# Optimization experiments

Measured on AMD Instinct MI355X. Metric: run time of the kernel, lower is better.

The kernel has to match this reference:

```python
import jax, jax.numpy as jnp
import numpy as np

N = 100000   # nodes
E = 1600000  # edges (before self-loops)
D = 128      # input_dim
H = 128      # hidden_dim


def setup_inputs() -> dict:
    key = jax.random.key(0)
    ks = jax.random.split(key, 10)
    def lin_w(k, fan_in, fan_out):
        return jax.random.normal(k, (fan_in, fan_out), jnp.float32) / np.float32(np.sqrt(fan_in))
    x = jax.random.normal(ks[0], (N, D), jnp.float32)
    edge_index = jax.random.randint(ks[1], (2, E), 0, N)
    return {
        "x": x,
        "edge_index": edge_index,
        "W0": lin_w(ks[2], D, H), "b0": jnp.zeros((H,), jnp.float32),
        "W1": lin_w(ks[3], H, H), "b1": jnp.zeros((H,), jnp.float32),
        "W2": lin_w(ks[4], H, H), "b2": jnp.zeros((H,), jnp.float32),
        "Wr": lin_w(ks[5], D, H), "br": jnp.zeros((H,), jnp.float32),
    }


def _gcn_norm(edge_index, n):
    # add self-loops, then symmetric normalization D^{-1/2} (A+I) D^{-1/2}
    loop = jnp.arange(n, dtype=edge_index.dtype)
    src = jnp.concatenate([edge_index[0], loop])
    dst = jnp.concatenate([edge_index[1], loop])
    deg = jax.ops.segment_sum(jnp.ones_like(src, dtype=jnp.float32), dst, num_segments=n)
    dinv = jnp.where(deg > 0, jax.lax.rsqrt(deg), 0.0)
    norm = dinv[src] * dinv[dst]  # [E+N]
    return src, dst, norm


def _gcn_layer(x, W, b, src, dst, norm, n):
    h = x @ W                      # [n, H] dense GEMM
    msg = h[src] * norm[:, None]   # gather + scale  [E+N, H]
    out = jax.ops.segment_sum(msg, dst, num_segments=n)  # scatter-add
    return out + b


def reference(x, edge_index, W0, b0, W1, b1, W2, b2, Wr, br):
    n = x.shape[0]
    src, dst, norm = _gcn_norm(edge_index, n)
    residual = x @ Wr + br
    # layer 0: GCN -> relu -> (dropout=identity, eval) -> +residual
    h = jax.nn.relu(_gcn_layer(x, W0, b0, src, dst, norm, n)) + residual
    # layer 1
    h = jax.nn.relu(_gcn_layer(h, W1, b1, src, dst, norm, n))
    # layer 2
    h = jax.nn.relu(_gcn_layer(h, W2, b2, src, dst, norm, n))
    return h
```

## Files before the change

kernel.cpp:

```cpp
#include <hip/hip_runtime.h>
#include <hip/hip_bf16.h>
#include <cstdint>


#define WS_ALIGN(x) (((x) + 255) & ~(size_t)255)

typedef __bf16 bf16x8 __attribute__((ext_vector_type(8)));
typedef float  floatx4 __attribute__((ext_vector_type(4)));

static __device__ __forceinline__ float bf_lo(unsigned u) {
  return __builtin_bit_cast(float, u << 16);
}
static __device__ __forceinline__ float bf_hi(unsigned u) {
  return __builtin_bit_cast(float, u & 0xffff0000u);
}
static __device__ __forceinline__ unsigned short f2bs(float f) {
  unsigned u = __builtin_bit_cast(unsigned, f);
  return (unsigned short)((u + 0x7fffu + ((u >> 16) & 1u)) >> 16);
}
static __device__ __forceinline__ unsigned pack2(float a, float b) {
  return (unsigned)f2bs(a) | ((unsigned)f2bs(b) << 16);
}

__global__ void k_prep(const float* __restrict__ x, unsigned* __restrict__ xb, int n4,
                       int* __restrict__ cnt, int n,
                       const float* __restrict__ W0, const float* __restrict__ W1,
                       const float* __restrict__ W2, const float* __restrict__ Wr,
                       unsigned short* __restrict__ Wt, int zb, int xbn) {
  int b = blockIdx.x;
  if (b < zb) {
    int i = b * 256 + threadIdx.x;
    if (i < n) cnt[i] = 0;
  } else if (b < zb + xbn) {
    int i = (b - zb) * 256 + threadIdx.x;
    if (i < n4) {
      float4 v = ((const float4*)x)[i];
      uint2 o;
      o.x = pack2(v.x, v.y);
      o.y = pack2(v.z, v.w);
      ((uint2*)xb)[i] = o;
    }
  } else {
    int wb = b - zb - xbn;
    int mat = wb >> 6, blk = wb & 63;
    const float* W = mat == 0 ? W0 : mat == 1 ? W1 : mat == 2 ? W2 : Wr;
    unsigned short* T = Wt + (size_t)mat * 16384;
    int i = blk * 256 + threadIdx.x;
    int k = i >> 7, nn = i & 127;
    T[nn * 128 + k] = f2bs(W[i]);
  }
}

__global__ void k_count(const int* __restrict__ dst, int E,
                        int* __restrict__ cnt, int* __restrict__ pos) {
  int e = blockIdx.x * blockDim.x + threadIdx.x;
  if (e < E) pos[e] = atomicAdd(&cnt[dst[e]], 1);
}

__global__ __launch_bounds__(1024) void k_scan1(const int* __restrict__ cnt, int n,
                                                int* __restrict__ rs, int* __restrict__ bsum,
                                                float* __restrict__ dinv) {
  __shared__ int tmp[1024];
  int tid = threadIdx.x;
  int i = blockIdx.x * 1024 + tid;
  int v = (i < n) ? cnt[i] : 0;
  if (i < n) dinv[i] = rsqrtf((float)(v + 1));
  int vp = (v + 7) & ~7;
  tmp[tid] = vp;
  __syncthreads();
  for (int off = 1; off < 1024; off <<= 1) {
    int t = (tid >= off) ? tmp[tid - off] : 0;
    __syncthreads();
    tmp[tid] += t;
    __syncthreads();
  }
  if (i < n) rs[i] = tmp[tid] - vp;
  if (tid == 1023) bsum[blockIdx.x] = tmp[1023];
}

__global__ __launch_bounds__(128) void k_scan2(int* bsum, int nb) {
  __shared__ int tmp[128];
  int tid = threadIdx.x;
  int v = (tid < nb) ? bsum[tid] : 0;
  tmp[tid] = v;
  __syncthreads();
  for (int off = 1; off < 128; off <<= 1) {
    int t = (tid >= off) ? tmp[tid - off] : 0;
    __syncthreads();
    tmp[tid] += t;
    __syncthreads();
  }
  if (tid < nb) bsum[tid] = tmp[tid] - v;
}

__global__ void k_fill(const int* __restrict__ src, const int* __restrict__ dst, int E,
                       const int* __restrict__ rs, const int* __restrict__ bsum,
                       const int* __restrict__ pos, const int* __restrict__ cnt,
                       const float* __restrict__ dinv,
                       int2* __restrict__ epk, int n) {
  int e = blockIdx.x * blockDim.x + threadIdx.x;
  if (e < E) {
    int s = src[e], d = dst[e];
    int idx = rs[d] + bsum[d >> 10] + pos[e];
    int2 v;
    v.x = s;
    v.y = __float_as_int(dinv[s] * dinv[d]);
    epk[idx] = v;
  } else if (e - E < n) {
    int node = e - E;
    int c = cnt[node];
    int cp = (c + 7) & ~7;
    int base = rs[node] + bsum[node >> 10];
    int2 z; z.x = 0; z.y = 0;
    for (int k = base + c; k < base + cp; k++) epk[k] = z;
  }
}

__global__ __launch_bounds__(256, 2) void k_gemm_mfma(
    const unsigned short* __restrict__ Xb,
    const unsigned short* __restrict__ Wt,
    const float* __restrict__ bias,
    unsigned short* __restrict__ Y,
    int n) {
  __shared__ unsigned short sWt[128 * 128];
  {
    const uint4* s4 = (const uint4*)Wt;
    uint4* d4 = (uint4*)sWt;
    for (int i = threadIdx.x; i < 2048; i += 256) d4[i] = s4[i];
  }
  __syncthreads();

  const int lane = threadIdx.x & 63;
  const int wave = threadIdx.x >> 6;
  const int l15 = lane & 15;
  const int quad = lane >> 4;
  const int rbase = blockIdx.x * 64 + wave * 16;

  const bf16x8* sW8 = (const bf16x8*)sWt;
  bf16x8 b[8][4];
#pragma unroll
  for (int ct = 0; ct < 8; ct++)
#pragma unroll
    for (int kc = 0; kc < 4; kc++)
      b[ct][kc] = sW8[(ct * 16 + l15) * 16 + kc * 4 + quad];

  int row = rbase + l15;
  row = row < n ? row : n - 1;
  const bf16x8* X8 = (const bf16x8*)Xb;
  bf16x8 a[4];
#pragma unroll
  for (int kc = 0; kc < 4; kc++)
    a[kc] = X8[(size_t)row * 16 + kc * 4 + quad];

  floatx4 acc[8];
#pragma unroll
  for (int ct = 0; ct < 8; ct++) acc[ct] = (floatx4){0.f, 0.f, 0.f, 0.f};

#pragma unroll
  for (int kc = 0; kc < 4; kc++)
#pragma unroll
    for (int ct = 0; ct < 8; ct++)
      acc[ct] = __builtin_amdgcn_mfma_f32_16x16x32_bf16(a[kc], b[ct][kc], acc[ct], 0, 0, 0);

  const int orow = rbase + quad * 4;
#pragma unroll
  for (int ct = 0; ct < 8; ct++) {
    const int c = ct * 16 + l15;
    const float bv = bias ? bias[c] : 0.f;
#pragma unroll
    for (int r4 = 0; r4 < 4; r4++) {
      int r = orow + r4;
      if (r < n) Y[(size_t)r * 128 + c] = f2bs(acc[ct][r4] + bv);
    }
  }
}

static __device__ __forceinline__ void fma8(float wgt, uint4 h, float* a) {
  a[0] = fmaf(wgt, bf_lo(h.x), a[0]);
  a[1] = fmaf(wgt, bf_hi(h.x), a[1]);
  a[2] = fmaf(wgt, bf_lo(h.y), a[2]);
  a[3] = fmaf(wgt, bf_hi(h.y), a[3]);
  a[4] = fmaf(wgt, bf_lo(h.z), a[4]);
  a[5] = fmaf(wgt, bf_hi(h.z), a[5]);
  a[6] = fmaf(wgt, bf_lo(h.w), a[6]);
  a[7] = fmaf(wgt, bf_hi(h.w), a[7]);
}

__global__ __launch_bounds__(256, 4) void k_agg(
    const uint4* __restrict__ H,
    const int* __restrict__ rs,
    const int* __restrict__ bsum,
    const int* __restrict__ cnt,
    const int2* __restrict__ epk,
    const float* __restrict__ dinv,
    const float* __restrict__ bias,
    const uint4* __restrict__ resid,
    uint4* __restrict__ outb,
    float4* __restrict__ outf,
    int n) {
  int node = blockIdx.x * 16 + (threadIdx.x >> 4);
  int l = threadIdx.x & 15;
  if (node >= n) return;

  float di = dinv[node];
  float ws = di * di;
  uint4 hv = H[(size_t)node * 16 + l];
  float a[8];
  a[0] = bf_lo(hv.x) * ws; a[1] = bf_hi(hv.x) * ws;
  a[2] = bf_lo(hv.y) * ws; a[3] = bf_hi(hv.y) * ws;
  a[4] = bf_lo(hv.z) * ws; a[5] = bf_hi(hv.z) * ws;
  a[6] = bf_lo(hv.w) * ws; a[7] = bf_hi(hv.w) * ws;

  int beg = rs[node] + bsum[node >> 10];
  int pdeg = (cnt[node] + 7) & ~7;
  const int4* epk4 = (const int4*)epk;

  for (int j = 0; j < pdeg; j += 8) {
    int b2 = (beg + j) >> 1;
    int4 e0 = epk4[b2 + 0];
    int4 e1 = epk4[b2 + 1];
    int4 e2 = epk4[b2 + 2];
    int4 e3 = epk4[b2 + 3];
    uint4 h0 = H[(size_t)(unsigned)e0.x * 16 + l];
    uint4 h1 = H[(size_t)(unsigned)e0.z * 16 + l];
    uint4 h2 = H[(size_t)(unsigned)e1.x * 16 + l];
    uint4 h3 = H[(size_t)(unsigned)e1.z * 16 + l];
    uint4 h4 = H[(size_t)(unsigned)e2.x * 16 + l];
    uint4 h5 = H[(size_t)(unsigned)e2.z * 16 + l];
    uint4 h6 = H[(size_t)(unsigned)e3.x * 16 + l];
    uint4 h7 = H[(size_t)(unsigned)e3.z * 16 + l];
    fma8(__int_as_float(e0.y), h0, a);
    fma8(__int_as_float(e0.w), h1, a);
    fma8(__int_as_float(e1.y), h2, a);
    fma8(__int_as_float(e1.w), h3, a);
    fma8(__int_as_float(e2.y), h4, a);
    fma8(__int_as_float(e2.w), h5, a);
    fma8(__int_as_float(e3.y), h6, a);
    fma8(__int_as_float(e3.w), h7, a);
  }

  float4 bl = ((const float4*)bias)[l * 2];
  float4 bh = ((const float4*)bias)[l * 2 + 1];
  a[0] = fmaxf(a[0] + bl.x, 0.f); a[1] = fmaxf(a[1] + bl.y, 0.f);
  a[2] = fmaxf(a[2] + bl.z, 0.f); a[3] = fmaxf(a[3] + bl.w, 0.f);
  a[4] = fmaxf(a[4] + bh.x, 0.f); a[5] = fmaxf(a[5] + bh.y, 0.f);
  a[6] = fmaxf(a[6] + bh.z, 0.f); a[7] = fmaxf(a[7] + bh.w, 0.f);
  if (resid) {
    uint4 r = resid[(size_t)node * 16 + l];
    a[0] += bf_lo(r.x); a[1] += bf_hi(r.x);
    a[2] += bf_lo(r.y); a[3] += bf_hi(r.y);
    a[4] += bf_lo(r.z); a[5] += bf_hi(r.z);
    a[6] += bf_lo(r.w); a[7] += bf_hi(r.w);
  }
  if (outb) {
    uint4 o;
    o.x = pack2(a[0], a[1]); o.y = pack2(a[2], a[3]);
    o.z = pack2(a[4], a[5]); o.w = pack2(a[6], a[7]);
    outb[(size_t)node * 16 + l] = o;
  } else {
    float4 o0; o0.x = a[0]; o0.y = a[1]; o0.z = a[2]; o0.w = a[3];
    float4 o1; o1.x = a[4]; o1.y = a[5]; o1.z = a[6]; o1.w = a[7];
    outf[(size_t)node * 32 + l * 2] = o0;
    outf[(size_t)node * 32 + l * 2 + 1] = o1;
  }
}

extern "C" void kernel_launch(void* const* d_in, const int* in_sizes, int n_in,
                              void* d_out, int out_size, void* d_ws, size_t ws_size,
                              hipStream_t stream) {
  const float* x  = (const float*)d_in[0];
  const int* edges = (const int*)d_in[1];
  const float* W0 = (const float*)d_in[2];
  const float* b0 = (const float*)d_in[3];
  const float* W1 = (const float*)d_in[4];
  const float* b1 = (const float*)d_in[5];
  const float* W2 = (const float*)d_in[6];
  const float* b2 = (const float*)d_in[7];
  const float* Wr = (const float*)d_in[8];
  const float* br = (const float*)d_in[9];

  int N = in_sizes[0] / 128;
  int E = in_sizes[1] / 2;
  const int* src = edges;
  const int* dst = edges + E;

  char* ws = (char*)d_ws;
  size_t off = 0;
  auto alloc = [&](size_t bytes) -> void* {
    void* p = ws + off; off = WS_ALIGN(off + bytes); return p;
  };
  int*   cnt    = (int*)  alloc((size_t)N * 4);
  float* dinv   = (float*)alloc((size_t)N * 4);
  int*   rs     = (int*)  alloc((size_t)(N + 1) * 4);
  int*   bsum   = (int*)  alloc(1024);
  int2*  epk    = (int2*) alloc(((size_t)E + 8 * (size_t)N) * 8);
  unsigned short* xb = (unsigned short*)alloc((size_t)N * 128 * 2);
  unsigned short* Wt = (unsigned short*)alloc((size_t)4 * 16384 * 2);
  unsigned short* A  = (unsigned short*)alloc((size_t)N * 128 * 2);
  unsigned short* Hb = (unsigned short*)alloc((size_t)N * 128 * 2);
  unsigned short* R  = (unsigned short*)alloc((size_t)N * 128 * 2);
  int* pos = (int*)A;
  (void)ws_size; (void)n_in; (void)out_size;

  int nb1 = (N + 1023) / 1024;

  int n4 = N * 128 / 4;
  int zb = (N + 255) / 256;
  int xbn = (n4 + 255) / 256;
  k_prep <<<zb + xbn + 256, 256, 0, stream>>>(x, (unsigned*)xb, n4, cnt, N,
                                              W0, W1, W2, Wr, Wt, zb, xbn);
  k_count<<<(E + 255) / 256, 256, 0, stream>>>(dst, E, cnt, pos);
  k_scan1<<<nb1, 1024, 0, stream>>>(cnt, N, rs, bsum, dinv);
  k_scan2<<<1, 128, 0, stream>>>(bsum, nb1);
  k_fill <<<(E + N + 255) / 256, 256, 0, stream>>>(src, dst, E, rs, bsum, pos,
                                                   cnt, dinv, epk, N);

  int gb = (N + 63) / 64;
  int ab = (N + 15) / 16;

  unsigned short* Wt0 = Wt;
  unsigned short* Wt1 = Wt + 16384;
  unsigned short* Wt2 = Wt + 2 * 16384;
  unsigned short* Wtr = Wt + 3 * 16384;

  k_gemm_mfma<<<gb, 256, 0, stream>>>(xb, Wtr, br, R, N);
  k_gemm_mfma<<<gb, 256, 0, stream>>>(xb, Wt0, nullptr, A, N);
  k_agg<<<ab, 256, 0, stream>>>((const uint4*)A, rs, bsum, cnt, epk, dinv, b0,
                                (const uint4*)R, (uint4*)Hb, nullptr, N);
  k_gemm_mfma<<<gb, 256, 0, stream>>>(Hb, Wt1, nullptr, A, N);
  k_agg<<<ab, 256, 0, stream>>>((const uint4*)A, rs, bsum, cnt, epk, dinv, b1,
                                nullptr, (uint4*)R, nullptr, N);
  k_gemm_mfma<<<gb, 256, 0, stream>>>(R, Wt2, nullptr, A, N);
  k_agg<<<ab, 256, 0, stream>>>((const uint4*)A, rs, bsum, cnt, epk, dinv, b2,
                                nullptr, nullptr, (float4*)d_out, N);
}
```

Baseline: 526.4 us.

## Privatize per-XCC degree counters to avoid cross-die atomic contention in CSR build

The edge-count kernel now reads the hardware XCC id and increments one of eight per-XCC copies of the destination counters with workgroup-scope relaxed atomics. It stores the rank together with the XCC id in pos. The scan kernel folds the eight copies into per-XCC offsets and a total degree. The fill kernel combines these to place each edge. The intent is to keep counting atomics inside each XCC's L2 and avoid device-coherent traffic, at the cost of eight times the counter memory (aliased onto the Hb buffer) plus the extra scan and fill reads; the workgroup-scope atomic is only correct if L2 coherence within an XCC holds across workgroups.

```diff
diff --git a/kernel.cpp b/kernel.cpp
--- a/kernel.cpp
+++ b/kernel.cpp
@@ -23,14 +23,14 @@
 }
 
 __global__ void k_prep(const float* __restrict__ x, unsigned* __restrict__ xb, int n4,
-                       int* __restrict__ cnt, int n,
+                       int* __restrict__ cnt8, int nz,
                        const float* __restrict__ W0, const float* __restrict__ W1,
                        const float* __restrict__ W2, const float* __restrict__ Wr,
                        unsigned short* __restrict__ Wt, int zb, int xbn) {
   int b = blockIdx.x;
   if (b < zb) {
     int i = b * 256 + threadIdx.x;
-    if (i < n) cnt[i] = 0;
+    if (i < nz) cnt8[i] = 0;
   } else if (b < zb + xbn) {
     int i = (b - zb) * 256 + threadIdx.x;
     if (i < n4) {
@@ -52,26 +52,46 @@
 }
 
 __global__ void k_count(const int* __restrict__ dst, int E,
-                        int* __restrict__ cnt, int* __restrict__ pos) {
+                        int* __restrict__ cnt8, int* __restrict__ pos, int NP) {
+  unsigned xcc = __builtin_amdgcn_s_getreg(6164);
+  int r = xcc & 7;
   int e = blockIdx.x * blockDim.x + threadIdx.x;
-  if (e < E) pos[e] = atomicAdd(&cnt[dst[e]], 1);
-}
-
-__global__ __launch_bounds__(1024) void k_scan1(const int* __restrict__ cnt, int n,
+  if (e < E) {
+    int d = dst[e];
+    int rank = __hip_atomic_fetch_add(&cnt8[(size_t)r * NP + d], 1,
+                                      __ATOMIC_RELAXED, __HIP_MEMORY_SCOPE_WORKGROUP);
+    pos[e] = (rank << 3) | r;
+  }
+}
+
+__global__ __launch_bounds__(1024) void k_scan1(int* __restrict__ cnt8, int n, int NP,
                                                 int* __restrict__ rs, int* __restrict__ bsum,
-                                                float* __restrict__ dinv) {
+                                                float* __restrict__ dinv,
+                                                int* __restrict__ tot) {
   __shared__ int tmp[1024];
   int tid = threadIdx.x;
   int i = blockIdx.x * 1024 + tid;
-  int v = (i < n) ? cnt[i] : 0;
-  if (i < n) dinv[i] = rsqrtf((float)(v + 1));
-  int vp = (v + 7) & ~7;
+  int t = 0;
+  if (i < n) {
+    int run = 0;
+#pragma unroll
+    for (int r = 0; r < 8; r++) {
+      size_t idx = (size_t)r * NP + i;
+      int c = cnt8[idx];
+      cnt8[idx] = run;
+      run += c;
+    }
+    t = run;
+    tot[i] = t;
+    dinv[i] = rsqrtf((float)(t + 1));
+  }
+  int vp = (t + 7) & ~7;
   tmp[tid] = vp;
   __syncthreads();
   for (int off = 1; off < 1024; off <<= 1) {
-    int t = (tid >= off) ? tmp[tid - off] : 0;
+    int tv = (tid >= off) ? tmp[tid - off] : 0;
     __syncthreads();
-    tmp[tid] += t;
+    tmp[tid] += tv;
     __syncthreads();
   }
   if (i < n) rs[i] = tmp[tid] - vp;
@@ -95,20 +115,22 @@
 
 __global__ void k_fill(const int* __restrict__ src, const int* __restrict__ dst, int E,
                        const int* __restrict__ rs, const int* __restrict__ bsum,
-                       const int* __restrict__ pos, const int* __restrict__ cnt,
+                       const int* __restrict__ pos, const int* __restrict__ cnt8,
+                       const int* __restrict__ tot, int NP,
                        const float* __restrict__ dinv,
                        int2* __restrict__ epk, int n) {
   int e = blockIdx.x * blockDim.x + threadIdx.x;
   if (e < E) {
     int s = src[e], d = dst[e];
-    int idx = rs[d] + bsum[d >> 10] + pos[e];
+    int pr = pos[e];
+    int idx = rs[d] + bsum[d >> 10] + cnt8[(size_t)(pr & 7) * NP + d] + (pr >> 3);
     int2 v;
     v.x = s;
     v.y = __float_as_int(dinv[s] * dinv[d]);
     epk[idx] = v;
   } else if (e - E < n) {
     int node = e - E;
-    int c = cnt[node];
+    int c = tot[node];
     int cp = (c + 7) & ~7;
     int base = rs[node] + bsum[node >> 10];
     int2 z; z.x = 0; z.y = 0;
@@ -190,7 +212,7 @@
     const uint4* __restrict__ H,
     const int* __restrict__ rs,
     const int* __restrict__ bsum,
-    const int* __restrict__ cnt,
+    const int* __restrict__ tot,
     const int2* __restrict__ epk,
     const float* __restrict__ dinv,
     const float* __restrict__ bias,
@@ -212,7 +234,7 @@
   a[6] = bf_lo(hv.w) * ws; a[7] = bf_hi(hv.w) * ws;
 
   int beg = rs[node] + bsum[node >> 10];
-  int pdeg = (cnt[node] + 7) & ~7;
+  int pdeg = (tot[node] + 7) & ~7;
   const int4* epk4 = (const int4*)epk;
 
   for (int j = 0; j < pdeg; j += 8) {
@@ -289,7 +311,7 @@
   auto alloc = [&](size_t bytes) -> void* {
     void* p = ws + off; off = WS_ALIGN(off + bytes); return p;
   };
-  int*   cnt    = (int*)  alloc((size_t)N * 4);
+  int*   tot    = (int*)  alloc((size_t)N * 4);
   float* dinv   = (float*)alloc((size_t)N * 4);
   int*   rs     = (int*)  alloc((size_t)(N + 1) * 4);
   int*   bsum   = (int*)  alloc(1024);
@@ -300,20 +322,23 @@
   unsigned short* Hb = (unsigned short*)alloc((size_t)N * 128 * 2);
   unsigned short* R  = (unsigned short*)alloc((size_t)N * 128 * 2);
   int* pos = (int*)A;
+  int NP = (N + 15) & ~15;
+  int* cnt8 = (int*)Hb;
+  int nz = 8 * NP;
   (void)ws_size; (void)n_in; (void)out_size;
 
   int nb1 = (N + 1023) / 1024;
 
   int n4 = N * 128 / 4;
-  int zb = (N + 255) / 256;
+  int zb = (nz + 255) / 256;
   int xbn = (n4 + 255) / 256;
-  k_prep <<<zb + xbn + 256, 256, 0, stream>>>(x, (unsigned*)xb, n4, cnt, N,
+  k_prep <<<zb + xbn + 256, 256, 0, stream>>>(x, (unsigned*)xb, n4, cnt8, nz,
                                               W0, W1, W2, Wr, Wt, zb, xbn);
-  k_count<<<(E + 255) / 256, 256, 0, stream>>>(dst, E, cnt, pos);
-  k_scan1<<<nb1, 1024, 0, stream>>>(cnt, N, rs, bsum, dinv);
+  k_count<<<(E + 255) / 256, 256, 0, stream>>>(dst, E, cnt8, pos, NP);
+  k_scan1<<<nb1, 1024, 0, stream>>>(cnt8, N, NP, rs, bsum, dinv, tot);
   k_scan2<<<1, 128, 0, stream>>>(bsum, nb1);
   k_fill <<<(E + N + 255) / 256, 256, 0, stream>>>(src, dst, E, rs, bsum, pos,
-                                                   cnt, dinv, epk, N);
+                                                   cnt8, tot, NP, dinv, epk, N);
 
   int gb = (N + 63) / 64;
   int ab = (N + 15) / 16;
@@ -325,12 +350,12 @@
 
   k_gemm_mfma<<<gb, 256, 0, stream>>>(xb, Wtr, br, R, N);
   k_gemm_mfma<<<gb, 256, 0, stream>>>(xb, Wt0, nullptr, A, N);
-  k_agg<<<ab, 256, 0, stream>>>((const uint4*)A, rs, bsum, cnt, epk, dinv, b0,
+  k_agg<<<ab, 256, 0, stream>>>((const uint4*)A, rs, bsum, tot, epk, dinv, b0,
                                 (const uint4*)R, (uint4*)Hb, nullptr, N);
   k_gemm_mfma<<<gb, 256, 0, stream>>>(Hb, Wt1, nullptr, A, N);
-  k_agg<<<ab, 256, 0, stream>>>((const uint4*)A, rs, bsum, cnt, epk, dinv, b1,
+  k_agg<<<ab, 256, 0, stream>>>((const uint4*)A, rs, bsum, tot, epk, dinv, b1,
                                 nullptr, (uint4*)R, nullptr, N);
   k_gemm_mfma<<<gb, 256, 0, stream>>>(R, Wt2, nullptr, A, N);
-  k_agg<<<ab, 256, 0, stream>>>((const uint4*)A, rs, bsum, cnt, epk, dinv, b2,
+  k_agg<<<ab, 256, 0, stream>>>((const uint4*)A, rs, bsum, tot, epk, dinv, b2,
                                 nullptr, nullptr, (float4*)d_out, N);
 }
```

Result: no change. 527.3 us (+0.2%).

## Replace CSR build with fixed-slot adjacency plus overflow list and prescaled features

Applied to the files above, without the earlier changes.

Replaces the count/scan/fill CSR construction with a single atomic pass that writes each edge's source into a 32-slot per-node array, spilling extra edges to a global overflow list. The symmetric normalization is factored: the GEMM epilogue scales each row by dinv[src] and the aggregation applies dinv[dst] at the end, so edges store only indices and the inner loop becomes plain adds. Padding slots point at a zeroed dummy row N. This removes three launches and the 8-byte edge records, but high-degree nodes linearly scan the whole overflow list, and neighbor order now depends on atomic ordering.

```diff
diff --git a/kernel.cpp b/kernel.cpp
--- a/kernel.cpp
+++ b/kernel.cpp
@@ -26,7 +26,9 @@
                        int* __restrict__ cnt, int n,
                        const float* __restrict__ W0, const float* __restrict__ W1,
                        const float* __restrict__ W2, const float* __restrict__ Wr,
-                       unsigned short* __restrict__ Wt, int zb, int xbn) {
+                       unsigned short* __restrict__ Wt,
+                       unsigned short* __restrict__ A, int* __restrict__ ovfn,
+                       int zb, int xbn) {
   int b = blockIdx.x;
   if (b < zb) {
     int i = b * 256 + threadIdx.x;
@@ -42,77 +44,20 @@
     }
   } else {
     int wb = b - zb - xbn;
-    int mat = wb >> 6, blk = wb & 63;
-    const float* W = mat == 0 ? W0 : mat == 1 ? W1 : mat == 2 ? W2 : Wr;
-    unsigned short* T = Wt + (size_t)mat * 16384;
-    int i = blk * 256 + threadIdx.x;
-    int k = i >> 7, nn = i & 127;
-    T[nn * 128 + k] = f2bs(W[i]);
-  }
-}
-
-__global__ void k_count(const int* __restrict__ dst, int E,
-                        int* __restrict__ cnt, int* __restrict__ pos) {
-  int e = blockIdx.x * blockDim.x + threadIdx.x;
-  if (e < E) pos[e] = atomicAdd(&cnt[dst[e]], 1);
-}
-
-__global__ __launch_bounds__(1024) void k_scan1(const int* __restrict__ cnt, int n,
-                                                int* __restrict__ rs, int* __restrict__ bsum,
-                                                float* __restrict__ dinv) {
-  __shared__ int tmp[1024];
-  int tid = threadIdx.x;
-  int i = blockIdx.x * 1024 + tid;
-  int v = (i < n) ? cnt[i] : 0;
-  if (i < n) dinv[i] = rsqrtf((float)(v + 1));
-  int vp = (v + 7) & ~7;
-  tmp[tid] = vp;
-  __syncthreads();
-  for (int off = 1; off < 1024; off <<= 1) {
-    int t = (tid >= off) ? tmp[tid - off] : 0;
-    __syncthreads();
-    tmp[tid] += t;
-    __syncthreads();
-  }
-  if (i < n) rs[i] = tmp[tid] - vp;
-  if (tid == 1023) bsum[blockIdx.x] = tmp[1023];
-}
-
-__global__ __launch_bounds__(128) void k_scan2(int* bsum, int nb) {
-  __shared__ int tmp[128];
-  int tid = threadIdx.x;
-  int v = (tid < nb) ? bsum[tid] : 0;
-  tmp[tid] = v;
-  __syncthreads();
-  for (int off = 1; off < 128; off <<= 1) {
-    int t = (tid >= off) ? tmp[tid - off] : 0;
-    __syncthreads();
-    tmp[tid] += t;
-    __syncthreads();
-  }
-  if (tid < nb) bsum[tid] = tmp[tid] - v;
-}
-
-__global__ void k_fill(const int* __restrict__ src, const int* __restrict__ dst, int E,
-                       const int* __restrict__ rs, const int* __restrict__ bsum,
-                       const int* __restrict__ pos, const int* __restrict__ cnt,
-                       const float* __restrict__ dinv,
-                       int2* __restrict__ epk, int n) {
-  int e = blockIdx.x * blockDim.x + threadIdx.x;
-  if (e < E) {
-    int s = src[e], d = dst[e];
-    int idx = rs[d] + bsum[d >> 10] + pos[e];
-    int2 v;
-    v.x = s;
-    v.y = __float_as_int(dinv[s] * dinv[d]);
-    epk[idx] = v;
-  } else if (e - E < n) {
-    int node = e - E;
-    int c = cnt[node];
-    int cp = (c + 7) & ~7;
-    int base = rs[node] + bsum[node >> 10];
-    int2 z; z.x = 0; z.y = 0;
-    for (int k = base + c; k < base + cp; k++) epk[k] = z;
+    if (wb < 256) {
+      int mat = wb >> 6, blk = wb & 63;
+      const float* W = mat == 0 ? W0 : mat == 1 ? W1 : mat == 2 ? W2 : Wr;
+      unsigned short* T = Wt + (size_t)mat * 16384;
+      int i = blk * 256 + threadIdx.x;
+      int k = i >> 7, nn = i & 127;
+      T[nn * 128 + k] = f2bs(W[i]);
+    } else {
+      if (threadIdx.x < 16) {
+        uint4 z; z.x = 0; z.y = 0; z.z = 0; z.w = 0;
+        ((uint4*)(A + (size_t)n * 128))[threadIdx.x] = z;
+      }
+      if (threadIdx.x == 16) *ovfn = 0;
+    }
   }
 }
 
@@ -120,6 +65,7 @@
     const unsigned short* __restrict__ Xb,
     const unsigned short* __restrict__ Wt,
     const float* __restrict__ bias,
+    const float* __restrict__ dv,
     unsigned short* __restrict__ Y,
     int n) {
   __shared__ unsigned short sWt[128 * 128];
@@ -163,6 +109,12 @@
       acc[ct] = __builtin_amdgcn_mfma_f32_16x16x32_bf16(a[kc], b[ct][kc], acc[ct], 0, 0, 0);
 
   const int orow = rbase + quad * 4;
+  float4 dvv;
+  dvv.x = 1.f; dvv.y = 1.f; dvv.z = 1.f; dvv.w = 1.f;
+  if (dv) {
+    int od = orow < n ? orow : 0;
+    dvv = *(const float4*)(dv + od);
+  }
 #pragma unroll
   for (int ct = 0; ct < 8; ct++) {
     const int c = ct * 16 + l15;
@@ -170,81 +122,107 @@
 #pragma unroll
     for (int r4 = 0; r4 < 4; r4++) {
       int r = orow + r4;
-      if (r < n) Y[(size_t)r * 128 + c] = f2bs(acc[ct][r4] + bv);
-    }
-  }
-}
-
-static __device__ __forceinline__ void fma8(float wgt, uint4 h, float* a) {
-  a[0] = fmaf(wgt, bf_lo(h.x), a[0]);
-  a[1] = fmaf(wgt, bf_hi(h.x), a[1]);
-  a[2] = fmaf(wgt, bf_lo(h.y), a[2]);
-  a[3] = fmaf(wgt, bf_hi(h.y), a[3]);
-  a[4] = fmaf(wgt, bf_lo(h.z), a[4]);
-  a[5] = fmaf(wgt, bf_hi(h.z), a[5]);
-  a[6] = fmaf(wgt, bf_lo(h.w), a[6]);
-  a[7] = fmaf(wgt, bf_hi(h.w), a[7]);
+      float dm = r4 == 0 ? dvv.x : r4 == 1 ? dvv.y : r4 == 2 ? dvv.z : dvv.w;
+      if (r < n) Y[(size_t)r * 128 + c] = f2bs(acc[ct][r4] * dm + bv);
+    }
+  }
+}
+
+__global__ void k_fill1p(const int* __restrict__ srcv, const int* __restrict__ dstv,
+                         int E, int* __restrict__ cnt, int* __restrict__ epk,
+                         int2* __restrict__ ovf, int* __restrict__ ovfn) {
+  int e = blockIdx.x * blockDim.x + threadIdx.x;
+  if (e < E) {
+    int s = srcv[e], d = dstv[e];
+    int rank = atomicAdd(&cnt[d], 1);
+    if (rank < 32) {
+      epk[(size_t)d * 32 + rank] = s;
+    } else {
+      int o = atomicAdd(ovfn, 1);
+      if (o < E) {
+        int2 t; t.x = s; t.y = d;
+        ovf[o] = t;
+      }
+    }
+  }
+}
+
+__global__ void k_aux(const int* __restrict__ cnt, float* __restrict__ dinv,
+                      int* __restrict__ epk, int n) {
+  int i = blockIdx.x * 256 + threadIdx.x;
+  if (i < n) {
+    int c = cnt[i];
+    dinv[i] = rsqrtf((float)(c + 1));
+    int cm = c < 32 ? c : 32;
+    int cp = (cm + 7) & ~7;
+    for (int k = cm; k < cp; k++) epk[(size_t)i * 32 + k] = n;
+  }
+}
+
+static __device__ __forceinline__ void add8(uint4 h, float* a) {
+  a[0] += bf_lo(h.x); a[1] += bf_hi(h.x);
+  a[2] += bf_lo(h.y); a[3] += bf_hi(h.y);
+  a[4] += bf_lo(h.z); a[5] += bf_hi(h.z);
+  a[6] += bf_lo(h.w); a[7] += bf_hi(h.w);
 }
 
 __global__ __launch_bounds__(256, 4) void k_agg(
     const uint4* __restrict__ H,
-    const int* __restrict__ rs,
-    const int* __restrict__ bsum,
     const int* __restrict__ cnt,
-    const int2* __restrict__ epk,
+    const int* __restrict__ epk,
     const float* __restrict__ dinv,
     const float* __restrict__ bias,
     const uint4* __restrict__ resid,
     uint4* __restrict__ outb,
     float4* __restrict__ outf,
-    int n) {
+    const int2* __restrict__ ovf, const int* __restrict__ ovfn,
+    int n, int Ecap) {
   int node = blockIdx.x * 16 + (threadIdx.x >> 4);
   int l = threadIdx.x & 15;
   if (node >= n) return;
 
-  float di = dinv[node];
-  float ws = di * di;
+  int tot = cnt[node];
+  int cm = tot < 32 ? tot : 32;
+  int pdeg = (cm + 7) & ~7;
+
   uint4 hv = H[(size_t)node * 16 + l];
   float a[8];
-  a[0] = bf_lo(hv.x) * ws; a[1] = bf_hi(hv.x) * ws;
-  a[2] = bf_lo(hv.y) * ws; a[3] = bf_hi(hv.y) * ws;
-  a[4] = bf_lo(hv.z) * ws; a[5] = bf_hi(hv.z) * ws;
-  a[6] = bf_lo(hv.w) * ws; a[7] = bf_hi(hv.w) * ws;
-
-  int beg = rs[node] + bsum[node >> 10];
-  int pdeg = (cnt[node] + 7) & ~7;
-  const int4* epk4 = (const int4*)epk;
-
+  a[0] = bf_lo(hv.x); a[1] = bf_hi(hv.x);
+  a[2] = bf_lo(hv.y); a[3] = bf_hi(hv.y);
+  a[4] = bf_lo(hv.z); a[5] = bf_hi(hv.z);
+  a[6] = bf_lo(hv.w); a[7] = bf_hi(hv.w);
+
+  const int4* epk4 = (const int4*)(epk + (size_t)node * 32);
   for (int j = 0; j < pdeg; j += 8) {
-    int b2 = (beg + j) >> 1;
-    int4 e0 = epk4[b2 + 0];
-    int4 e1 = epk4[b2 + 1];
-    int4 e2 = epk4[b2 + 2];
-    int4 e3 = epk4[b2 + 3];
+    int4 e0 = epk4[j >> 2];
+    int4 e1 = epk4[(j >> 2) + 1];
     uint4 h0 = H[(size_t)(unsigned)e0.x * 16 + l];
-    uint4 h1 = H[(size_t)(unsigned)e0.z * 16 + l];
-    uint4 h2 = H[(size_t)(unsigned)e1.x * 16 + l];
-    uint4 h3 = H[(size_t)(unsigned)e1.z * 16 + l];
-    uint4 h4 = H[(size_t)(unsigned)e2.x * 16 + l];
-    uint4 h5 = H[(size_t)(unsigned)e2.z * 16 + l];
-    uint4 h6 = H[(size_t)(unsigned)e3.x * 16 + l];
-    uint4 h7 = H[(size_t)(unsigned)e3.z * 16 + l];
-    fma8(__int_as_float(e0.y), h0, a);
-    fma8(__int_as_float(e0.w), h1, a);
-    fma8(__int_as_float(e1.y), h2, a);
-    fma8(__int_as_float(e1.w), h3, a);
-    fma8(__int_as_float(e2.y), h4, a);
-    fma8(__int_as_float(e2.w), h5, a);
-    fma8(__int_as_float(e3.y), h6, a);
-    fma8(__int_as_float(e3.w), h7, a);
-  }
-
+    uint4 h1 = H[(size_t)(unsigned)e0.y * 16 + l];
+    uint4 h2 = H[(size_t)(unsigned)e0.z * 16 + l];
+    uint4 h3 = H[(size_t)(unsigned)e0.w * 16 + l];
+    uint4 h4 = H[(size_t)(unsigned)e1.x * 16 + l];
+    uint4 h5 = H[(size_t)(unsigned)e1.y * 16 + l];
+    uint4 h6 = H[(size_t)(unsigned)e1.z * 16 + l];
+    uint4 h7 = H[(size_t)(unsigned)e1.w * 16 + l];
+    add8(h0, a); add8(h1, a); add8(h2, a); add8(h3, a);
+    add8(h4, a); add8(h5, a); add8(h6, a); add8(h7, a);
+  }
+  if (tot > 32) {
+    int no = *ovfn;
+    no = no < Ecap ? no : Ecap;
+    for (int i = 0; i < no; i++) {
+      int2 t = ovf[i];
+      if (t.y == node) add8(H[(size_t)(unsigned)t.x * 16 + l], a);
+    }
+  }
+
+  float dn = dinv[node];
   float4 bl = ((const float4*)bias)[l * 2];
   float4 bh = ((const float4*)bias)[l * 2 + 1];
-  a[0] = fmaxf(a[0] + bl.x, 0.f); a[1] = fmaxf(a[1] + bl.y, 0.f);
-  a[2] = fmaxf(a[2] + bl.z, 0.f); a[3] = fmaxf(a[3] + bl.w, 0.f);
-  a[4] = fmaxf(a[4] + bh.x, 0.f); a[5] = fmaxf(a[5] + bh.y, 0.f);
-  a[6] = fmaxf(a[6] + bh.z, 0.f); a[7] = fmaxf(a[7] + bh.w, 0.f);
+  a[0] = fmaxf(fmaf(a[0], dn, bl.x), 0.f); a[1] = fmaxf(fmaf(a[1], dn, bl.y), 0.f);
+  a[2] = fmaxf(fmaf(a[2], dn, bl.z), 0.f); a[3] = fmaxf(fmaf(a[3], dn, bl.w), 0.f);
+  a[4] = fmaxf(fmaf(a[4], dn, bh.x), 0.f); a[5] = fmaxf(fmaf(a[5], dn, bh.y), 0.f);
+  a[6] = fmaxf(fmaf(a[6], dn, bh.z), 0.f); a[7] = fmaxf(fmaf(a[7], dn, bh.w), 0.f);
   if (resid) {
     uint4 r = resid[(size_t)node * 16 + l];
     a[0] += bf_lo(r.x); a[1] += bf_hi(r.x);
@@ -289,48 +267,43 @@
   auto alloc = [&](size_t bytes) -> void* {
     void* p = ws + off; off = WS_ALIGN(off + bytes); return p;
   };
-  int*   cnt    = (int*)  alloc((size_t)N * 4);
-  float* dinv   = (float*)alloc((size_t)N * 4);
-  int*   rs     = (int*)  alloc((size_t)(N + 1) * 4);
-  int*   bsum   = (int*)  alloc(1024);
-  int2*  epk    = (int2*) alloc(((size_t)E + 8 * (size_t)N) * 8);
+  int*   cnt  = (int*)  alloc((size_t)N * 4);
+  float* dinv = (float*)alloc((size_t)N * 4);
+  int*   ovfn = (int*)  alloc(256);
+  int2*  ovf  = (int2*) alloc((size_t)E * 8);
+  int*   epk  = (int*)  alloc((size_t)N * 32 * 4);
   unsigned short* xb = (unsigned short*)alloc((size_t)N * 128 * 2);
   unsigned short* Wt = (unsigned short*)alloc((size_t)4 * 16384 * 2);
-  unsigned short* A  = (unsigned short*)alloc((size_t)N * 128 * 2);
+  unsigned short* A  = (unsigned short*)alloc(((size_t)N + 1) * 128 * 2);
   unsigned short* Hb = (unsigned short*)alloc((size_t)N * 128 * 2);
   unsigned short* R  = (unsigned short*)alloc((size_t)N * 128 * 2);
-  int* pos = (int*)A;
   (void)ws_size; (void)n_in; (void)out_size;
-
-  int nb1 = (N + 1023) / 1024;
 
   int n4 = N * 128 / 4;
   int zb = (N + 255) / 256;
   int xbn = (n4 + 255) / 256;
-  k_prep <<<zb + xbn + 256, 256, 0, stream>>>(x, (unsigned*)xb, n4, cnt, N,
-                                              W0, W1, W2, Wr, Wt, zb, xbn);
-  k_count<<<(E + 255) / 256, 256, 0, stream>>>(dst, E, cnt, pos);
-  k_scan1<<<nb1, 1024, 0, stream>>>(cnt, N, rs, bsum, dinv);
-  k_scan2<<<1, 128, 0, stream>>>(bsum, nb1);
-  k_fill <<<(E + N + 255) / 256, 256, 0, stream>>>(src, dst, E, rs, bsum, pos,
-                                                   cnt, dinv, epk, N);
+  k_prep<<<zb + xbn + 257, 256, 0, stream>>>(x, (unsigned*)xb, n4, cnt, N,
+                                             W0, W1, W2, Wr, Wt, A, ovfn, zb, xbn);
 
   int gb = (N + 63) / 64;
-  int ab = (N + 15) / 16;
-
+  int eb = (E + 255) / 256;
   unsigned short* Wt0 = Wt;
   unsigned short* Wt1 = Wt + 16384;
   unsigned short* Wt2 = Wt + 2 * 16384;
   unsigned short* Wtr = Wt + 3 * 16384;
-
-  k_gemm_mfma<<<gb, 256, 0, stream>>>(xb, Wtr, br, R, N);
-  k_gemm_mfma<<<gb, 256, 0, stream>>>(xb, Wt0, nullptr, A, N);
-  k_agg<<<ab, 256, 0, stream>>>((const uint4*)A, rs, bsum, cnt, epk, dinv, b0,
-                                (const uint4*)R, (uint4*)Hb, nullptr, N);
-  k_gemm_mfma<<<gb, 256, 0, stream>>>(Hb, Wt1, nullptr, A, N);
-  k_agg<<<ab, 256, 0, stream>>>((const uint4*)A, rs, bsum, cnt, epk, dinv, b1,
-                                nullptr, (uint4*)R, nullptr, N);
-  k_gemm_mfma<<<gb, 256, 0, stream>>>(R, Wt2, nullptr, A, N);
-  k_agg<<<ab, 256, 0, stream>>>((const uint4*)A, rs, bsum, cnt, epk, dinv, b2,
-                                nullptr, nullptr, (float4*)d_out, N);
-}
+  k_fill1p<<<eb, 256, 0, stream>>>(src, dst, E, cnt, epk, ovf, ovfn);
+  k_gemm_mfma<<<gb, 256, 0, stream>>>(xb, Wtr, br, nullptr, R, N);
+  k_aux<<<(N + 255) / 256, 256, 0, stream>>>(cnt, dinv, epk, N);
+
+  int ab = (N + 15) / 16;
+
+  k_gemm_mfma<<<gb, 256, 0, stream>>>(xb, Wt0, nullptr, dinv, A, N);
+  k_agg<<<ab, 256, 0, stream>>>((const uint4*)A, cnt, epk, dinv, b0,
+                                (const uint4*)R, (uint4*)Hb, nullptr, ovf, ovfn, N, E);
+  k_gemm_mfma<<<gb, 256, 0, stream>>>(Hb, Wt1, nullptr, dinv, A, N);
+  k_agg<<<ab, 256, 0, stream>>>((const uint4*)A, cnt, epk, dinv, b1,
+                                nullptr, (uint4*)R, nullptr, ovf, ovfn, N, E);
+  k_gemm_mfma<<<gb, 256, 0, stream>>>(R, Wt2, nullptr, dinv, A, N);
+  k_agg<<<ab, 256, 0, stream>>>((const uint4*)A, cnt, epk, dinv, b2,
+                                nullptr, nullptr, (float4*)d_out, ovf, ovfn, N, E);
+}
```

Result: faster. 515.0 us (-2.2%).
